# Kernel optimization log

Hardware: AMD Instinct MI355X
Metric: run time of the kernel (lower is better)

## Reference

```python
import jax, jax.numpy as jnp
import numpy as np

B, S, H, DH, E = 8, 2048, 1024, 4096, 8
ALPHA = 0.5
LN_EPS = 1e-5


def setup_inputs() -> dict:
    key = jax.random.key(0)
    ks = jax.random.split(key, 8)
    sc = 0.02
    return {
        "x": jax.random.normal(ks[0], (B, S, H), jnp.float32),
        "We1": jax.random.normal(ks[1], (E, H, DH), jnp.float32) * sc,
        "be1": jnp.zeros((E, DH), jnp.float32),
        "We2": jax.random.normal(ks[2], (E, DH, H), jnp.float32) * sc,
        "be2": jnp.zeros((E, H), jnp.float32),
        "Wq": jax.random.normal(ks[3], (H, H), jnp.float32) * sc,
        "bq": jnp.zeros((H,), jnp.float32),
        "Wk": jax.random.normal(ks[4], (H, H), jnp.float32) * sc,
        "bk": jnp.zeros((H,), jnp.float32),
        "Wv": jax.random.normal(ks[5], (H, H), jnp.float32) * sc,
        "bv": jnp.zeros((H,), jnp.float32),
        "ln_g": jnp.ones((H,), jnp.float32),
        "ln_b": jnp.zeros((H,), jnp.float32),
        "current_expert_idx": E - 1,
    }


def _boosting_forward(x, We1, be1, We2, be2, Wq, bq, Wk, bk, Wv, bv, ln_g, ln_b, cur):
    sg = jax.lax.stop_gradient
    n = cur + 1  # static Python int: number of experts executed
    boost = sg(x)  # boost_input = x.detach()
    outs = []
    for i in range(n):
        h = jax.nn.relu(jnp.einsum("bsh,hf->bsf", boost, We1[i]) + be1[i])
        eo = jnp.einsum("bsf,fh->bsh", h, We2[i]) + be2[i]  # dropout = identity (eval)
        if i < n - 1:
            eo = sg(eo)  # earlier experts detached
        boost = boost + ALPHA * eo
        outs.append(eo)
    stacked = jnp.stack(outs, axis=2)  # [B,S,n,H]
    q = jnp.einsum("bsh,hd->bsd", x, Wq) + bq          # [B,S,H]
    k = jnp.einsum("bseh,hd->bsed", stacked, Wk) + bk  # [B,S,n,H]
    v = jnp.einsum("bseh,hd->bsed", stacked, Wv) + bv
    scores = jnp.einsum("bsd,bsed->bse", q, k) / jnp.sqrt(jnp.asarray(H, x.dtype))
    w = jax.nn.softmax(scores, axis=-1)                # [B,S,n]
    fused = jnp.einsum("bse,bsed->bsd", w, v)          # [B,S,H]
    y = x + fused
    mu = jnp.mean(y, axis=-1, keepdims=True)
    var = jnp.mean(jnp.square(y - mu), axis=-1, keepdims=True)
    return (y - mu) * jax.lax.rsqrt(var + LN_EPS) * ln_g + ln_b


def reference(x, We1, be1, We2, be2, Wq, bq, Wk, bk, Wv, bv, ln_g, ln_b, current_expert_idx):
    return _boosting_forward(x, We1, be1, We2, be2, Wq, bq, Wk, bk, Wv, bv, ln_g, ln_b, int(current_expert_idx))
```

## Files before the change

### kernel.cpp

```cpp
#include <hip/hip_runtime.h>
#include <math.h>

typedef __bf16 bf16_t;
typedef __bf16 bf16x8 __attribute__((ext_vector_type(8)));
typedef __bf16 bf16x4 __attribute__((ext_vector_type(4)));
typedef float f32x4 __attribute__((ext_vector_type(4)));
typedef unsigned int u32;

static constexpr int kBd = 8, kS = 2048, kH = 1024, kDH = 4096, kE = 8;
static constexpr int kM = kBd * kS;
static constexpr float kScale = 0.03125f;

__device__ __forceinline__ void gload_lds16(const void* g, void* l) {
  __builtin_amdgcn_global_load_lds(
      (const __attribute__((address_space(1))) u32*)g,
      (__attribute__((address_space(3))) u32*)l, 16, 0, 0);
}

__global__ __launch_bounds__(256) void cvt_flat_kernel(const float* __restrict__ in,
                                                       bf16_t* __restrict__ out, int n4) {
  int i = blockIdx.x * 256 + threadIdx.x;
  if (i >= n4) return;
  f32x4 v = *(const f32x4*)(in + (size_t)i * 4);
  bf16x4 o;
#pragma unroll
  for (int j = 0; j < 4; ++j) o[j] = (bf16_t)v[j];
  *(bf16x4*)(out + (size_t)i * 4) = o;
}

__global__ __launch_bounds__(256) void transpose_cvt_kernel(
    const float* __restrict__ in, bf16_t* __restrict__ out, int R, int C) {
  __shared__ float tile[32][33];
  int tx = threadIdx.x & 31, ty = threadIdx.x >> 5;
  int c0 = blockIdx.x * 32, r0 = blockIdx.y * 32;
#pragma unroll
  for (int yy = 0; yy < 4; ++yy)
    tile[ty + yy * 8][tx] = in[(size_t)(r0 + ty + yy * 8) * C + c0 + tx];
  __syncthreads();
#pragma unroll
  for (int yy = 0; yy < 4; ++yy)
    out[(size_t)(c0 + ty + yy * 8) * R + r0 + tx] = (bf16_t)tile[tx][ty + yy * 8];
}

template <int MODE>
__global__ __launch_bounds__(512, 2) void gemm256_kernel(
    const bf16_t* __restrict__ A, const bf16_t* __restrict__ Bt,
    int M, int N, int K, int nwg,
    const float* __restrict__ bias,
    bf16_t* __restrict__ outb,
    const bf16_t* __restrict__ bin_b, bf16_t* __restrict__ bout_b,
    bf16_t* __restrict__ stacked,
    const float* __restrict__ xres, float* __restrict__ yout,
    const int* __restrict__ curp, int expert_i) {
  if ((MODE == 0 || MODE == 4) && expert_i > *curp) return;
  extern __shared__ char lds_buf[];
  char* Abase = lds_buf;
  char* Bbase = lds_buf + 98304;
  const int tid = threadIdx.x;
  const int lane = tid & 63, wid = tid >> 6;
  const int wr = wid >> 2, wc = wid & 3;
  const int fr = lane & 15, fh = lane >> 4;
  const int lane_swz = (fr * 64 + fh * 16) ^ ((fr >> 3) << 5);
  const int bid = blockIdx.x;
  const int wg = (bid & 7) * (nwg >> 3) + (bid >> 3);
  const int nNb = N >> 8;
  const int chsz = 8 * nNb;
  const int chunk = wg / chsz, loc = wg % chsz;
  const int m0 = (chunk * 8 + (loc & 7)) << 8;
  const int n0 = (loc >> 3) << 8;
  int grow[2], gcol[2];
#pragma unroll
  for (int j = 0; j < 2; ++j) {
    int L = (j * 512 + tid) * 16;
    int Lp = L ^ (((L >> 9) & 1) << 5);
    int s = Lp >> 10;
    grow[j] = ((s >> 1) << 4) + ((Lp >> 6) & 15);
    gcol[j] = ((s & 1) << 5) + (((Lp >> 4) & 3) << 3);
  }
  const bf16_t* sA[2] = {A + (size_t)(m0 + grow[0]) * K + gcol[0],
                         A + (size_t)(m0 + grow[1]) * K + gcol[1]};
  const bf16_t* sB[2] = {Bt + (size_t)(n0 + grow[0]) * K + gcol[0],
                         Bt + (size_t)(n0 + grow[1]) * K + gcol[1]};
  const size_t rstep = (size_t)128 * K;

#define STAGE(SP, BASE, tau, h)                                               \
  {                                                                           \
    char* d_ = (BASE) + ((h) << 14) + (wid << 10);                            \
    gload_lds16(SP[0] + (size_t)(h)*rstep + (size_t)(tau)*64, d_);            \
    gload_lds16(SP[1] + (size_t)(h)*rstep + (size_t)(tau)*64, d_ + 8192);     \
  }
#define STAGE_A(buf, t, h) STAGE(sA, Abase + (buf)*32768, (t), (h))
#define STAGE_B(t, h) STAGE(sB, Bbase + (((t)&1) << 15), (t), (h))
#define SB0() __builtin_amdgcn_sched_barrier(0)

  const int bq = (wc & 1) * 4;

  f32x4 acc[8][4] = {};
  const int NT = K >> 6;

#define QUAD(p, af)                                                            \
  __builtin_amdgcn_s_setprio(1);                                               \
  _Pragma("unroll") for (int nf = 0; nf < 4; ++nf) {                           \
    acc[2 * (p)][nf] = __builtin_amdgcn_mfma_f32_16x16x32_bf16(                \
        af[0], b[nf][0], acc[2 * (p)][nf], 0, 0, 0);                           \
    acc[2 * (p)][nf] = __builtin_amdgcn_mfma_f32_16x16x32_bf16(                \
        af[1], b[nf][1], acc[2 * (p)][nf], 0, 0, 0);                           \
    acc[2 * (p) + 1][nf] = __builtin_amdgcn_mfma_f32_16x16x32_bf16(            \
        af[2], b[nf][0], acc[2 * (p) + 1][nf], 0, 0, 0);                       \
    acc[2 * (p) + 1][nf] = __builtin_amdgcn_mfma_f32_16x16x32_bf16(            \
        af[3], b[nf][1], acc[2 * (p) + 1][nf], 0, 0, 0);                       \
  }                                                                            \
  __builtin_amdgcn_s_setprio(0);

  STAGE_A(0, 0, 0); STAGE_A(0, 0, 1);
  STAGE_B(0, 0); STAGE_B(0, 1);
  STAGE_A(1, 1, 0); STAGE_A(1, 1, 1);
  STAGE_B(1, 0); STAGE_B(1, 1);
  asm volatile("s_waitcnt vmcnt(8)" ::: "memory");
  __builtin_amdgcn_s_barrier();

  int am0 = 0;
  for (int t = 0; t < NT; ++t) {
    int am2 = am0 + 2; if (am2 >= 3) am2 -= 3;
    const char* Ar = Abase + am0 * 32768 + (wr << 14) + lane_swz;
    const char* Br = Bbase + ((t & 1) << 15) + ((wc >> 1) << 14) + lane_swz;
    bf16x8 b[4][2], a01[8], a23[8];
    const bool st = (t + 2 < NT);
#pragma unroll
    for (int nf = 0; nf < 4; ++nf)
#pragma unroll
      for (int kk = 0; kk < 2; ++kk)
        b[nf][kk] = *(const bf16x8*)(Br + ((bq + nf) * 2 + kk) * 1024);
    SB0();
#pragma unroll
    for (int i = 0; i < 8; ++i) a01[i] = *(const bf16x8*)(Ar + i * 1024);
    SB0();
    if (st) { STAGE_A(am2, t + 2, 0); STAGE_A(am2, t + 2, 1); }
    SB0();
    QUAD(0, (&a01[0]));
#pragma unroll
    for (int i = 0; i < 8; ++i) a23[i] = *(const bf16x8*)(Ar + (8 + i) * 1024);
    SB0();
    QUAD(1, (&a01[4]));
    asm volatile("s_waitcnt lgkmcnt(8)" ::: "memory");
    SB0();
    if (st) { STAGE_B(t + 2, 0); STAGE_B(t + 2, 1); }
    SB0();
    QUAD(2, (&a23[0]));
    QUAD(3, (&a23[4]));
    if (t < NT - 2) {
      asm volatile("s_waitcnt vmcnt(8)" ::: "memory");
    } else {
      asm volatile("s_waitcnt vmcnt(0)" ::: "memory");
    }
    __builtin_amdgcn_s_barrier();
    am0 = am0 + 1; if (am0 >= 3) am0 -= 3;
  }
#undef QUAD
#undef STAGE
#undef STAGE_A
#undef STAGE_B
#undef SB0

#pragma unroll
  for (int nf = 0; nf < 4; ++nf) {
    const int col = n0 + wc * 64 + nf * 16 + fr;
    const float bv = bias ? bias[col] : 0.0f;
#pragma unroll
    for (int mf = 0; mf < 8; ++mf) {
#pragma unroll
      for (int r = 0; r < 4; ++r) {
        const int row = m0 + wr * 128 + mf * 16 + fh * 4 + r;
        const size_t idx = (size_t)row * N + col;
        float v = acc[mf][nf][r] + bv;
        if (MODE == 0) {
          outb[idx] = (bf16_t)(v > 0.0f ? v : 0.0f);
        } else if (MODE == 2) {
          outb[idx] = (bf16_t)v;
        } else if (MODE == 4) {
          float nb2 = (float)bin_b[idx] + 0.5f * v;
          bout_b[idx] = (bf16_t)nb2;
          stacked[idx] = (bf16_t)v;
        } else {
          yout[idx] = v + xres[idx];
        }
      }
    }
  }
}

__global__ __launch_bounds__(256) void scores_mix_kernel(
    const bf16_t* __restrict__ qk, const bf16_t* __restrict__ q,
    const float* __restrict__ bk, const bf16_t* __restrict__ stacked,
    bf16_t* __restrict__ mix, const int* __restrict__ curp) {
  const int n = *curp + 1;
  int lane = threadIdx.x & 63, wave = threadIdx.x >> 6;
  int m = blockIdx.x * 4 + wave;
  size_t base = (size_t)m * kH + lane * 16;
  int c0 = lane * 16;
  bf16x8 qk0 = *(const bf16x8*)(qk + base);
  bf16x8 qk1 = *(const bf16x8*)(qk + base + 8);
  bf16x8 q0 = *(const bf16x8*)(q + base);
  bf16x8 q1 = *(const bf16x8*)(q + base + 8);
  float sc[kE + 1];
  bf16x8 eo0[kE], eo1[kE];
#pragma unroll
  for (int e = 0; e < kE; ++e) {
    sc[e] = 0.0f;
    if (e < n) {
      size_t sb = (size_t)e * kM * kH + base;
      eo0[e] = *(const bf16x8*)(stacked + sb);
      eo1[e] = *(const bf16x8*)(stacked + sb + 8);
      float d = 0.0f;
#pragma unroll
      for (int j = 0; j < 8; ++j)
        d += (float)eo0[e][j] * (float)qk0[j] + (float)eo1[e][j] * (float)qk1[j];
      sc[e] = d;
    }
  }
  {
    float qb = 0.0f;
#pragma unroll
    for (int j = 0; j < 8; ++j)
      qb += (float)q0[j] * bk[c0 + j] + (float)q1[j] * bk[c0 + 8 + j];
    sc[kE] = qb;
  }
#pragma unroll
  for (int off = 32; off >= 1; off >>= 1)
#pragma unroll
    for (int e = 0; e <= kE; ++e) sc[e] += __shfl_xor(sc[e], off, 64);
  float s[kE];
  float mx = -1e30f;
#pragma unroll
  for (int e = 0; e < kE; ++e)
    if (e < n) {
      s[e] = (sc[e] + sc[kE]) * kScale;
      mx = fmaxf(mx, s[e]);
    }
  float Z = 0.0f;
#pragma unroll
  for (int e = 0; e < kE; ++e)
    if (e < n) {
      s[e] = expf(s[e] - mx);
      Z += s[e];
    }
  float inv = 1.0f / Z;
  float mv[16];
#pragma unroll
  for (int j = 0; j < 16; ++j) mv[j] = 0.0f;
#pragma unroll
  for (int e = 0; e < kE; ++e)
    if (e < n) {
      float w = s[e] * inv;
#pragma unroll
      for (int j = 0; j < 8; ++j) {
        mv[j] += w * (float)eo0[e][j];
        mv[8 + j] += w * (float)eo1[e][j];
      }
    }
  bf16x8 o0, o1;
#pragma unroll
  for (int j = 0; j < 8; ++j) {
    o0[j] = (bf16_t)mv[j];
    o1[j] = (bf16_t)mv[8 + j];
  }
  *(bf16x8*)(mix + base) = o0;
  *(bf16x8*)(mix + base + 8) = o1;
}

__global__ __launch_bounds__(256) void layernorm_kernel(
    const float* __restrict__ y, const float* __restrict__ g,
    const float* __restrict__ b, float* __restrict__ out) {
  int lane = threadIdx.x & 63, wave = threadIdx.x >> 6;
  int m = blockIdx.x * 4 + wave;
  size_t base = (size_t)m * kH + lane * 16;
  f32x4 v[4];
#pragma unroll
  for (int j = 0; j < 4; ++j) v[j] = *(const f32x4*)(y + base + j * 4);
  float s = 0.0f, s2 = 0.0f;
#pragma unroll
  for (int j = 0; j < 4; ++j)
#pragma unroll
    for (int t = 0; t < 4; ++t) {
      float u = v[j][t];
      s += u;
      s2 += u * u;
    }
#pragma unroll
  for (int off = 32; off >= 1; off >>= 1) {
    s += __shfl_xor(s, off, 64);
    s2 += __shfl_xor(s2, off, 64);
  }
  float mu = s * (1.0f / kH);
  float var = s2 * (1.0f / kH) - mu * mu;
  float rs = rsqrtf(var + 1e-5f);
  int c0 = lane * 16;
#pragma unroll
  for (int j = 0; j < 4; ++j) {
    f32x4 gg = *(const f32x4*)(g + c0 + j * 4);
    f32x4 bb = *(const f32x4*)(b + c0 + j * 4);
    f32x4 o;
#pragma unroll
    for (int t = 0; t < 4; ++t) o[t] = (v[j][t] - mu) * rs * gg[t] + bb[t];
    *(f32x4*)(out + base + j * 4) = o;
  }
}

extern "C" void kernel_launch(void* const* d_in, const int* in_sizes, int n_in,
                              void* d_out, int out_size, void* d_ws, size_t ws_size,
                              hipStream_t stream) {
  const float* x = (const float*)d_in[0];
  const float* We1 = (const float*)d_in[1];
  const float* be1 = (const float*)d_in[2];
  const float* We2 = (const float*)d_in[3];
  const float* be2 = (const float*)d_in[4];
  const float* Wq = (const float*)d_in[5];
  const float* bq = (const float*)d_in[6];
  const float* Wk = (const float*)d_in[7];
  const float* bk = (const float*)d_in[8];
  const float* Wv = (const float*)d_in[9];
  const float* bv = (const float*)d_in[10];
  const float* ln_g = (const float*)d_in[11];
  const float* ln_b = (const float*)d_in[12];
  const int* curp = (const int*)d_in[13];
  float* out = (float*)d_out;

  char* ws = (char*)d_ws;
  const size_t MB = 1ull << 20;
  bf16_t* stacked = (bf16_t*)(ws);
  bf16_t* xb = (bf16_t*)(ws + 256 * MB);
  bf16_t* boostb = (bf16_t*)(ws + 288 * MB);
  bf16_t* wA = (bf16_t*)(ws + 320 * MB);
  bf16_t* wB = (bf16_t*)(ws + 328 * MB);
  bf16_t* WqT = (bf16_t*)(ws + 336 * MB);
  bf16_t* WkC = (bf16_t*)(ws + 338 * MB);
  bf16_t* WvT = (bf16_t*)(ws + 340 * MB);
  char* dyn = ws + 342 * MB;
  size_t rem = ws_size > 342 * MB ? ws_size - 342 * MB : 0;
  int nchunk;
  if (rem >= 128 * MB) nchunk = 1;
  else if (rem >= 64 * MB) nchunk = 2;
  else nchunk = 4;
  bf16_t* hbuf = (bf16_t*)dyn;
  bf16_t* qb_ = hbuf;
  bf16_t* qkb = boostb;
  bf16_t* mixb = xb;
  float* yf = (float*)ws;

  const int Mc = kM / nchunk;
  const size_t MH = (size_t)kM * kH;
  const u32 kLds = 163840;
  dim3 blk(256), blk5(512);

  cvt_flat_kernel<<<(kM * kH) / 1024, blk, 0, stream>>>(x, xb, (kM * kH) / 4);
  cvt_flat_kernel<<<(kH * kH) / 1024, blk, 0, stream>>>(Wk, WkC, (kH * kH) / 4);
  transpose_cvt_kernel<<<dim3(kH / 32, kH / 32), blk, 0, stream>>>(Wq, WqT, kH, kH);
  transpose_cvt_kernel<<<dim3(kH / 32, kH / 32), blk, 0, stream>>>(Wv, WvT, kH, kH);

  for (int i = 0; i < kE; ++i) {
    transpose_cvt_kernel<<<dim3(kDH / 32, kH / 32), blk, 0, stream>>>(
        We1 + (size_t)i * kH * kDH, wA, kH, kDH);
    transpose_cvt_kernel<<<dim3(kH / 32, kDH / 32), blk, 0, stream>>>(
        We2 + (size_t)i * kH * kDH, wB, kDH, kH);
    for (int c = 0; c < nchunk; ++c) {
      const size_t ro = (size_t)c * Mc * kH;
      const bf16_t* Ain = ((i == 0) ? xb : boostb) + ro;
      {
        int nwg = (Mc / 256) * (kDH / 256);
        gemm256_kernel<0><<<nwg, blk5, kLds, stream>>>(
            Ain, wA, Mc, kDH, kH, nwg, be1 + (size_t)i * kDH, hbuf,
            nullptr, nullptr, nullptr, nullptr, nullptr, curp, i);
      }
      int nwg = (Mc / 256) * (kH / 256);
      const bf16_t* binb = ((i == 0) ? xb : boostb) + ro;
      gemm256_kernel<4><<<nwg, blk5, kLds, stream>>>(
          hbuf, wB, Mc, kH, kDH, nwg, be2 + (size_t)i * kH, nullptr,
          binb, boostb + ro, stacked + (size_t)i * MH + ro,
          nullptr, nullptr, curp, i);
    }
  }

  const int nwgH = (kM / 256) * (kH / 256);
  gemm256_kernel<2><<<nwgH, blk5, kLds, stream>>>(
      xb, WqT, kM, kH, kH, nwgH, bq, qb_,
      nullptr, nullptr, nullptr, nullptr, nullptr, curp, 0);
  gemm256_kernel<2><<<nwgH, blk5, kLds, stream>>>(
      qb_, WkC, kM, kH, kH, nwgH, nullptr, qkb,
      nullptr, nullptr, nullptr, nullptr, nullptr, curp, 0);
  scores_mix_kernel<<<dim3(kM / 4), blk, 0, stream>>>(qkb, qb_, bk, stacked, mixb, curp);
  gemm256_kernel<3><<<nwgH, blk5, kLds, stream>>>(
      mixb, WvT, kM, kH, kH, nwgH, bv, nullptr,
      nullptr, nullptr, nullptr, x, yf, curp, 0);
  layernorm_kernel<<<dim3(kM / 4), blk, 0, stream>>>(yf, ln_g, ln_b, out);
}
```

Baseline: 2.898 ms.

## Prefetch B fragments across K-steps, stage epilogue through LDS, bf16 pre-LN output

The GEMM main loop is unrolled by two with ping-pong register buffers, so the next tile's B fragments are read from LDS during the current tile's MFMAs. The global-to-LDS staging order and vmcnt waits are adjusted to match. The epilogue now writes bf16 results into LDS first and then does coalesced 16-byte global stores, with boost/stacked/residual fused in vectorized form. The final GEMM writes the residual sum in bf16 instead of fp32, which halves that traffic but lowers the precision of the LayerNorm input.

```diff
diff --git a/kernel.cpp b/kernel.cpp
--- a/kernel.cpp
+++ b/kernel.cpp
@@ -50,7 +50,7 @@
     bf16_t* __restrict__ outb,
     const bf16_t* __restrict__ bin_b, bf16_t* __restrict__ bout_b,
     bf16_t* __restrict__ stacked,
-    const float* __restrict__ xres, float* __restrict__ yout,
+    const float* __restrict__ xres,
     const int* __restrict__ curp, int expert_i) {
   if ((MODE == 0 || MODE == 4) && expert_i > *curp) return;
   extern __shared__ char lds_buf[];
@@ -96,66 +96,81 @@
   const int bq = (wc & 1) * 4;
 
   f32x4 acc[8][4] = {};
+  bf16x8 b0[4][2], b1[4][2];
   const int NT = K >> 6;
 
-#define QUAD(p, af)                                                            \
+#define QUAD(p, B_, af)                                                        \
   __builtin_amdgcn_s_setprio(1);                                               \
   _Pragma("unroll") for (int nf = 0; nf < 4; ++nf) {                           \
     acc[2 * (p)][nf] = __builtin_amdgcn_mfma_f32_16x16x32_bf16(                \
-        af[0], b[nf][0], acc[2 * (p)][nf], 0, 0, 0);                           \
+        af[0], B_[nf][0], acc[2 * (p)][nf], 0, 0, 0);                          \
     acc[2 * (p)][nf] = __builtin_amdgcn_mfma_f32_16x16x32_bf16(                \
-        af[1], b[nf][1], acc[2 * (p)][nf], 0, 0, 0);                           \
+        af[1], B_[nf][1], acc[2 * (p)][nf], 0, 0, 0);                          \
     acc[2 * (p) + 1][nf] = __builtin_amdgcn_mfma_f32_16x16x32_bf16(            \
-        af[2], b[nf][0], acc[2 * (p) + 1][nf], 0, 0, 0);                       \
+        af[2], B_[nf][0], acc[2 * (p) + 1][nf], 0, 0, 0);                      \
     acc[2 * (p) + 1][nf] = __builtin_amdgcn_mfma_f32_16x16x32_bf16(            \
-        af[3], b[nf][1], acc[2 * (p) + 1][nf], 0, 0, 0);                       \
+        af[3], B_[nf][1], acc[2 * (p) + 1][nf], 0, 0, 0);                      \
   }                                                                            \
   __builtin_amdgcn_s_setprio(0);
 
+#define TILE(T, BIN, BNX)                                                      \
+  {                                                                            \
+    const int am2 = (am0 + 2 >= 3) ? am0 - 1 : am0 + 2;                        \
+    const char* Ar = Abase + am0 * 32768 + (wr << 14) + lane_swz;              \
+    const char* BrN =                                                          \
+        Bbase + ((((T) + 1) & 1) << 15) + ((wc >> 1) << 14) + lane_swz;        \
+    bf16x8 a01[8], a23[8];                                                     \
+    asm volatile("s_waitcnt lgkmcnt(0)" ::: "memory");                         \
+    SB0();                                                                     \
+    if ((T) + 2 < NT) { STAGE_B((T) + 2, 0); STAGE_B((T) + 2, 1); }            \
+    SB0();                                                                     \
+    _Pragma("unroll") for (int i = 0; i < 8; ++i)                              \
+        a01[i] = *(const bf16x8*)(Ar + i * 1024);                              \
+    SB0();                                                                     \
+    QUAD(0, BIN, (&a01[0]));                                                   \
+    _Pragma("unroll") for (int i = 0; i < 8; ++i)                              \
+        a23[i] = *(const bf16x8*)(Ar + (8 + i) * 1024);                        \
+    SB0();                                                                     \
+    QUAD(1, BIN, (&a01[4]));                                                   \
+    if ((T) + 1 < NT) {                                                        \
+      _Pragma("unroll") for (int nf = 0; nf < 4; ++nf)                         \
+          _Pragma("unroll") for (int kk = 0; kk < 2; ++kk)                     \
+          BNX[nf][kk] = *(const bf16x8*)(BrN + ((bq + nf) * 2 + kk) * 1024);   \
+    }                                                                          \
+    SB0();                                                                     \
+    if ((T) + 2 < NT) { STAGE_A(am2, (T) + 2, 0); STAGE_A(am2, (T) + 2, 1); }  \
+    SB0();                                                                     \
+    QUAD(2, BIN, (&a23[0]));                                                   \
+    QUAD(3, BIN, (&a23[4]));                                                   \
+    if ((T) < NT - 2)                                                          \
+      asm volatile("s_waitcnt vmcnt(4)" ::: "memory");                         \
+    else                                                                       \
+      asm volatile("s_waitcnt vmcnt(0)" ::: "memory");                         \
+    __builtin_amdgcn_s_barrier();                                              \
+    am0 = (am0 + 1 >= 3) ? 0 : am0 + 1;                                        \
+  }
+
   STAGE_A(0, 0, 0); STAGE_A(0, 0, 1);
   STAGE_B(0, 0); STAGE_B(0, 1);
+  STAGE_B(1, 0); STAGE_B(1, 1);
   STAGE_A(1, 1, 0); STAGE_A(1, 1, 1);
-  STAGE_B(1, 0); STAGE_B(1, 1);
-  asm volatile("s_waitcnt vmcnt(8)" ::: "memory");
+  asm volatile("s_waitcnt vmcnt(4)" ::: "memory");
   __builtin_amdgcn_s_barrier();
+  {
+    const char* Br0 = Bbase + ((wc >> 1) << 14) + lane_swz;
+#pragma unroll
+    for (int nf = 0; nf < 4; ++nf)
+#pragma unroll
+      for (int kk = 0; kk < 2; ++kk)
+        b0[nf][kk] = *(const bf16x8*)(Br0 + ((bq + nf) * 2 + kk) * 1024);
+  }
 
   int am0 = 0;
-  for (int t = 0; t < NT; ++t) {
-    int am2 = am0 + 2; if (am2 >= 3) am2 -= 3;
-    const char* Ar = Abase + am0 * 32768 + (wr << 14) + lane_swz;
-    const char* Br = Bbase + ((t & 1) << 15) + ((wc >> 1) << 14) + lane_swz;
-    bf16x8 b[4][2], a01[8], a23[8];
-    const bool st = (t + 2 < NT);
-#pragma unroll
-    for (int nf = 0; nf < 4; ++nf)
-#pragma unroll
-      for (int kk = 0; kk < 2; ++kk)
-        b[nf][kk] = *(const bf16x8*)(Br + ((bq + nf) * 2 + kk) * 1024);
-    SB0();
-#pragma unroll
-    for (int i = 0; i < 8; ++i) a01[i] = *(const bf16x8*)(Ar + i * 1024);
-    SB0();
-    if (st) { STAGE_A(am2, t + 2, 0); STAGE_A(am2, t + 2, 1); }
-    SB0();
-    QUAD(0, (&a01[0]));
-#pragma unroll
-    for (int i = 0; i < 8; ++i) a23[i] = *(const bf16x8*)(Ar + (8 + i) * 1024);
-    SB0();
-    QUAD(1, (&a01[4]));
-    asm volatile("s_waitcnt lgkmcnt(8)" ::: "memory");
-    SB0();
-    if (st) { STAGE_B(t + 2, 0); STAGE_B(t + 2, 1); }
-    SB0();
-    QUAD(2, (&a23[0]));
-    QUAD(3, (&a23[4]));
-    if (t < NT - 2) {
-      asm volatile("s_waitcnt vmcnt(8)" ::: "memory");
-    } else {
-      asm volatile("s_waitcnt vmcnt(0)" ::: "memory");
-    }
-    __builtin_amdgcn_s_barrier();
-    am0 = am0 + 1; if (am0 >= 3) am0 -= 3;
-  }
+  for (int t = 0; t < NT; t += 2) {
+    TILE(t, b0, b1);
+    TILE(t + 1, b1, b0);
+  }
+#undef TILE
 #undef QUAD
 #undef STAGE
 #undef STAGE_A
@@ -164,27 +179,45 @@
 
 #pragma unroll
   for (int nf = 0; nf < 4; ++nf) {
-    const int col = n0 + wc * 64 + nf * 16 + fr;
-    const float bv = bias ? bias[col] : 0.0f;
+    const int col = wc * 64 + nf * 16 + fr;
+    const float bv = bias ? bias[n0 + col] : 0.0f;
 #pragma unroll
     for (int mf = 0; mf < 8; ++mf) {
 #pragma unroll
       for (int r = 0; r < 4; ++r) {
-        const int row = m0 + wr * 128 + mf * 16 + fh * 4 + r;
-        const size_t idx = (size_t)row * N + col;
+        const int lrow = wr * 128 + mf * 16 + fh * 4 + r;
         float v = acc[mf][nf][r] + bv;
-        if (MODE == 0) {
-          outb[idx] = (bf16_t)(v > 0.0f ? v : 0.0f);
-        } else if (MODE == 2) {
-          outb[idx] = (bf16_t)v;
-        } else if (MODE == 4) {
-          float nb2 = (float)bin_b[idx] + 0.5f * v;
-          bout_b[idx] = (bf16_t)nb2;
-          stacked[idx] = (bf16_t)v;
-        } else {
-          yout[idx] = v + xres[idx];
-        }
+        if (MODE == 0) v = v > 0.0f ? v : 0.0f;
+        *(bf16_t*)(lds_buf + lrow * 516 + col * 2) = (bf16_t)v;
       }
+    }
+  }
+  __syncthreads();
+#pragma unroll
+  for (int i = 0; i < 16; ++i) {
+    const int lrow = i * 16 + (tid >> 5);
+    const int seg = tid & 31;
+    bf16x8 e = *(const bf16x8*)(lds_buf + lrow * 516 + seg * 16);
+    const size_t gi = (size_t)(m0 + lrow) * N + n0 + seg * 8;
+    if (MODE == 0 || MODE == 2) {
+      *(bf16x8*)(outb + gi) = e;
+    } else if (MODE == 4) {
+      bf16x8 bb = *(const bf16x8*)(bin_b + gi);
+      bf16x8 nb;
+#pragma unroll
+      for (int j = 0; j < 8; ++j) nb[j] = (bf16_t)((float)bb[j] + 0.5f * (float)e[j]);
+      *(bf16x8*)(bout_b + gi) = nb;
+      *(bf16x8*)(stacked + gi) = e;
+    } else {
+      f32x4 x0 = *(const f32x4*)(xres + gi);
+      f32x4 x1 = *(const f32x4*)(xres + gi + 4);
+      bf16x8 y;
+#pragma unroll
+      for (int j = 0; j < 4; ++j) {
+        y[j] = (bf16_t)((float)e[j] + x0[j]);
+        y[4 + j] = (bf16_t)((float)e[4 + j] + x1[j]);
+      }
+      *(bf16x8*)(outb + gi) = y;
     }
   }
 }
@@ -269,23 +302,25 @@
 }
 
 __global__ __launch_bounds__(256) void layernorm_kernel(
-    const float* __restrict__ y, const float* __restrict__ g,
+    const bf16_t* __restrict__ y, const float* __restrict__ g,
     const float* __restrict__ b, float* __restrict__ out) {
   int lane = threadIdx.x & 63, wave = threadIdx.x >> 6;
   int m = blockIdx.x * 4 + wave;
   size_t base = (size_t)m * kH + lane * 16;
-  f32x4 v[4];
-#pragma unroll
-  for (int j = 0; j < 4; ++j) v[j] = *(const f32x4*)(y + base + j * 4);
+  bf16x8 v0 = *(const bf16x8*)(y + base);
+  bf16x8 v1 = *(const bf16x8*)(y + base + 8);
   float s = 0.0f, s2 = 0.0f;
-#pragma unroll
-  for (int j = 0; j < 4; ++j)
-#pragma unroll
-    for (int t = 0; t < 4; ++t) {
-      float u = v[j][t];
-      s += u;
-      s2 += u * u;
-    }
+  float vf[16];
+#pragma unroll
+  for (int j = 0; j < 8; ++j) {
+    vf[j] = (float)v0[j];
+    vf[8 + j] = (float)v1[j];
+  }
+#pragma unroll
+  for (int j = 0; j < 16; ++j) {
+    s += vf[j];
+    s2 += vf[j] * vf[j];
+  }
 #pragma unroll
   for (int off = 32; off >= 1; off >>= 1) {
     s += __shfl_xor(s, off, 64);
@@ -301,7 +336,7 @@
     f32x4 bb = *(const f32x4*)(b + c0 + j * 4);
     f32x4 o;
 #pragma unroll
-    for (int t = 0; t < 4; ++t) o[t] = (v[j][t] - mu) * rs * gg[t] + bb[t];
+    for (int t = 0; t < 4; ++t) o[t] = (vf[j * 4 + t] - mu) * rs * gg[t] + bb[t];
     *(f32x4*)(out + base + j * 4) = o;
   }
 }
@@ -345,7 +380,7 @@
   bf16_t* qb_ = hbuf;
   bf16_t* qkb = boostb;
   bf16_t* mixb = xb;
-  float* yf = (float*)ws;
+  bf16_t* ybf = (bf16_t*)ws;
 
   const int Mc = kM / nchunk;
   const size_t MH = (size_t)kM * kH;
@@ -369,27 +404,26 @@
         int nwg = (Mc / 256) * (kDH / 256);
         gemm256_kernel<0><<<nwg, blk5, kLds, stream>>>(
             Ain, wA, Mc, kDH, kH, nwg, be1 + (size_t)i * kDH, hbuf,
-            nullptr, nullptr, nullptr, nullptr, nullptr, curp, i);
+            nullptr, nullptr, nullptr, nullptr, curp, i);
       }
       int nwg = (Mc / 256) * (kH / 256);
       const bf16_t* binb = ((i == 0) ? xb : boostb) + ro;
       gemm256_kernel<4><<<nwg, blk5, kLds, stream>>>(
           hbuf, wB, Mc, kH, kDH, nwg, be2 + (size_t)i * kH, nullptr,
-          binb, boostb + ro, stacked + (size_t)i * MH + ro,
-          nullptr, nullptr, curp, i);
+          binb, boostb + ro, stacked + (size_t)i * MH + ro, nullptr, curp, i);
     }
   }
 
   const int nwgH = (kM / 256) * (kH / 256);
   gemm256_kernel<2><<<nwgH, blk5, kLds, stream>>>(
       xb, WqT, kM, kH, kH, nwgH, bq, qb_,
-      nullptr, nullptr, nullptr, nullptr, nullptr, curp, 0);
+      nullptr, nullptr, nullptr, nullptr, curp, 0);
   gemm256_kernel<2><<<nwgH, blk5, kLds, stream>>>(
       qb_, WkC, kM, kH, kH, nwgH, nullptr, qkb,
-      nullptr, nullptr, nullptr, nullptr, nullptr, curp, 0);
+      nullptr, nullptr, nullptr, nullptr, curp, 0);
   scores_mix_kernel<<<dim3(kM / 4), blk, 0, stream>>>(qkb, qb_, bk, stacked, mixb, curp);
   gemm256_kernel<3><<<nwgH, blk5, kLds, stream>>>(
-      mixb, WvT, kM, kH, kH, nwgH, bv, nullptr,
-      nullptr, nullptr, nullptr, x, yf, curp, 0);
-  layernorm_kernel<<<dim3(kM / 4), blk, 0, stream>>>(yf, ln_g, ln_b, out);
-}
+      mixb, WvT, kM, kH, kH, nwgH, bv, ybf,
+      nullptr, nullptr, nullptr, x, curp, 0);
+  layernorm_kernel<<<dim3(kM / 4), blk, 0, stream>>>(ybf, ln_g, ln_b, out);
+}
```

Measured after the change: 3.523 ms. 1.22x slower.

## Prefetch next B fragments into ping-pong registers during GEMM main loop

Applied to the files above, without the earlier changes.

Splits the B-fragment registers into even and odd sets and unrolls the K loop by two. Each tile now reads the next tile's B fragments from LDS while it computes on the current ones. The B global->LDS stage is reordered to issue before the A stage, and the waitcnt thresholds change from vmcnt(8) to vmcnt(4). The aim is to hide LDS read latency for B behind the MFMA work, at the cost of more live VGPRs, which may hurt occupancy or cause spills.

```diff
diff --git a/kernel.cpp b/kernel.cpp
--- a/kernel.cpp
+++ b/kernel.cpp
@@ -96,66 +96,80 @@
   const int bq = (wc & 1) * 4;
 
   f32x4 acc[8][4] = {};
+  bf16x8 bE[4][2], bO[4][2];
   const int NT = K >> 6;
 
-#define QUAD(p, af)                                                            \
+#define QUAD(p, B_, af)                                                        \
   __builtin_amdgcn_s_setprio(1);                                               \
   _Pragma("unroll") for (int nf = 0; nf < 4; ++nf) {                           \
     acc[2 * (p)][nf] = __builtin_amdgcn_mfma_f32_16x16x32_bf16(                \
-        af[0], b[nf][0], acc[2 * (p)][nf], 0, 0, 0);                           \
+        af[0], B_[nf][0], acc[2 * (p)][nf], 0, 0, 0);                          \
     acc[2 * (p)][nf] = __builtin_amdgcn_mfma_f32_16x16x32_bf16(                \
-        af[1], b[nf][1], acc[2 * (p)][nf], 0, 0, 0);                           \
+        af[1], B_[nf][1], acc[2 * (p)][nf], 0, 0, 0);                          \
     acc[2 * (p) + 1][nf] = __builtin_amdgcn_mfma_f32_16x16x32_bf16(            \
-        af[2], b[nf][0], acc[2 * (p) + 1][nf], 0, 0, 0);                       \
+        af[2], B_[nf][0], acc[2 * (p) + 1][nf], 0, 0, 0);                      \
     acc[2 * (p) + 1][nf] = __builtin_amdgcn_mfma_f32_16x16x32_bf16(            \
-        af[3], b[nf][1], acc[2 * (p) + 1][nf], 0, 0, 0);                       \
+        af[3], B_[nf][1], acc[2 * (p) + 1][nf], 0, 0, 0);                      \
   }                                                                            \
   __builtin_amdgcn_s_setprio(0);
 
+#define TILE(T, BCUR, BNXT)                                                    \
+  {                                                                            \
+    int am2 = am0 + 2; if (am2 >= 3) am2 -= 3;                                 \
+    const char* Ar = Abase + am0 * 32768 + (wr << 14) + lane_swz;              \
+    const char* BrN =                                                          \
+        Bbase + ((((T) + 1) & 1) << 15) + ((wc >> 1) << 14) + lane_swz;        \
+    bf16x8 a01[8], a23[8];                                                     \
+    const bool st = ((T) + 2 < NT);                                            \
+    if (st) { STAGE_B((T) + 2, 0); STAGE_B((T) + 2, 1); }                      \
+    SB0();                                                                     \
+    _Pragma("unroll") for (int i = 0; i < 8; ++i)                              \
+        a01[i] = *(const bf16x8*)(Ar + i * 1024);                              \
+    SB0();                                                                     \
+    QUAD(0, BCUR, (&a01[0]));                                                  \
+    _Pragma("unroll") for (int i = 0; i < 8; ++i)                              \
+        a23[i] = *(const bf16x8*)(Ar + (8 + i) * 1024);                        \
+    SB0();                                                                     \
+    QUAD(1, BCUR, (&a01[4]));                                                  \
+    if ((T) + 1 < NT) {                                                        \
+      _Pragma("unroll") for (int nf = 0; nf < 4; ++nf)                         \
+          _Pragma("unroll") for (int kk = 0; kk < 2; ++kk)                     \
+          BNXT[nf][kk] = *(const bf16x8*)(BrN + ((bq + nf) * 2 + kk) * 1024);  \
+    }                                                                          \
+    SB0();                                                                     \
+    if (st) { STAGE_A(am2, (T) + 2, 0); STAGE_A(am2, (T) + 2, 1); }            \
+    SB0();                                                                     \
+    QUAD(2, BCUR, (&a23[0]));                                                  \
+    QUAD(3, BCUR, (&a23[4]));                                                  \
+    if ((T) < NT - 2)                                                          \
+      asm volatile("s_waitcnt vmcnt(4)" ::: "memory");                         \
+    else                                                                       \
+      asm volatile("s_waitcnt vmcnt(0)" ::: "memory");                         \
+    __builtin_amdgcn_s_barrier();                                              \
+    am0 = am0 + 1; if (am0 >= 3) am0 -= 3;                                     \
+  }
+
   STAGE_A(0, 0, 0); STAGE_A(0, 0, 1);
   STAGE_B(0, 0); STAGE_B(0, 1);
+  STAGE_B(1, 0); STAGE_B(1, 1);
   STAGE_A(1, 1, 0); STAGE_A(1, 1, 1);
-  STAGE_B(1, 0); STAGE_B(1, 1);
-  asm volatile("s_waitcnt vmcnt(8)" ::: "memory");
+  asm volatile("s_waitcnt vmcnt(4)" ::: "memory");
   __builtin_amdgcn_s_barrier();
+  {
+    const char* Br0 = Bbase + ((wc >> 1) << 14) + lane_swz;
+#pragma unroll
+    for (int nf = 0; nf < 4; ++nf)
+#pragma unroll
+      for (int kk = 0; kk < 2; ++kk)
+        bE[nf][kk] = *(const bf16x8*)(Br0 + ((bq + nf) * 2 + kk) * 1024);
+  }
 
   int am0 = 0;
-  for (int t = 0; t < NT; ++t) {
-    int am2 = am0 + 2; if (am2 >= 3) am2 -= 3;
-    const char* Ar = Abase + am0 * 32768 + (wr << 14) + lane_swz;
-    const char* Br = Bbase + ((t & 1) << 15) + ((wc >> 1) << 14) + lane_swz;
-    bf16x8 b[4][2], a01[8], a23[8];
-    const bool st = (t + 2 < NT);
-#pragma unroll
-    for (int nf = 0; nf < 4; ++nf)
-#pragma unroll
-      for (int kk = 0; kk < 2; ++kk)
-        b[nf][kk] = *(const bf16x8*)(Br + ((bq + nf) * 2 + kk) * 1024);
-    SB0();
-#pragma unroll
-    for (int i = 0; i < 8; ++i) a01[i] = *(const bf16x8*)(Ar + i * 1024);
-    SB0();
-    if (st) { STAGE_A(am2, t + 2, 0); STAGE_A(am2, t + 2, 1); }
-    SB0();
-    QUAD(0, (&a01[0]));
-#pragma unroll
-    for (int i = 0; i < 8; ++i) a23[i] = *(const bf16x8*)(Ar + (8 + i) * 1024);
-    SB0();
-    QUAD(1, (&a01[4]));
-    asm volatile("s_waitcnt lgkmcnt(8)" ::: "memory");
-    SB0();
-    if (st) { STAGE_B(t + 2, 0); STAGE_B(t + 2, 1); }
-    SB0();
-    QUAD(2, (&a23[0]));
-    QUAD(3, (&a23[4]));
-    if (t < NT - 2) {
-      asm volatile("s_waitcnt vmcnt(8)" ::: "memory");
-    } else {
-      asm volatile("s_waitcnt vmcnt(0)" ::: "memory");
-    }
-    __builtin_amdgcn_s_barrier();
-    am0 = am0 + 1; if (am0 >= 3) am0 -= 3;
-  }
+  for (int t = 0; t < NT; t += 2) {
+    TILE(t, bE, bO);
+    TILE(t + 1, bO, bE);
+  }
+#undef TILE
 #undef QUAD
 #undef STAGE
 #undef STAGE_A
```

Result: slower. 3.998 ms (+38.0%).
